# Kernel tuning notes

Measured on AMD Instinct MI355X. Metric: run time of the kernel, lower is better.

Reference implementation:

```python
import jax, jax.numpy as jnp
import numpy as np
from jax import lax

R = 1          # box-filter radius
EPS = 1e-06    # regularizer


def boxfilter(z, r=R):
    """ReplicationPad2d(r) + depthwise (groups=C) mean conv with kernel (2r+1)^2."""
    k = 2 * r + 1
    c = z.shape[1]
    zp = jnp.pad(z, ((0, 0), (0, 0), (r, r), (r, r)), mode='edge')  # replication pad
    w = jnp.full((c, 1, k, k), 1.0 / (k * k), dtype=z.dtype)        # [O, I/g, kh, kw]
    return lax.conv_general_dilated(zp, w, window_strides=(1, 1), padding='VALID',
                                    feature_group_count=c)


def setup_inputs() -> dict:
    key = jax.random.key(0)
    kx, ky = jax.random.split(key)
    shape = (8, 3, 1024, 1024)
    # image-valued inputs in [0, 255), matching the final clamp range
    x = jax.random.uniform(kx, shape, jnp.float32, 0.0, 255.0)
    y = jax.random.uniform(ky, shape, jnp.float32, 0.0, 255.0)
    return {"x": x, "y": y}


def reference(x, y):
    mean_x = boxfilter(x)
    mean_y = boxfilter(y)
    cov_xy = boxfilter(x * y) - mean_x * mean_y
    var_x = boxfilter(x * x) - mean_x * mean_x
    A = cov_xy / (var_x + EPS)
    b = mean_y - A * mean_x
    res = boxfilter(A) * x + boxfilter(b)
    # torch: res.int() truncates toward zero, clamp(0,255), back to float
    return jnp.clip(jnp.trunc(res), 0.0, 255.0)
```

## Files before the change

kernel.cpp:

```cpp
#include <hip/hip_runtime.h>


#define TW 64
#define TH 16

__global__ __launch_bounds__(256) void gf_kernel(
    const float* __restrict__ x, const float* __restrict__ y,
    float* __restrict__ out, int H, int W) {
  const int img = blockIdx.z;
  const size_t base = (size_t)img * H * W;
  const int tx0 = blockIdx.x * TW;
  const int ty0 = blockIdx.y * TH;

  __shared__ float sx[TH + 4][TW + 4];
  __shared__ float sy[TH + 4][TW + 4];
  __shared__ float sA[TH + 2][TW + 2];
  __shared__ float sB[TH + 2][TW + 2];

  const int tid = threadIdx.y * 64 + threadIdx.x;

  for (int i = tid; i < (TH + 4) * (TW + 4); i += 256) {
    int ly = i / (TW + 4);
    int lx = i - ly * (TW + 4);
    int gy = min(max(ty0 + ly - 2, 0), H - 1);
    int gx = min(max(tx0 + lx - 2, 0), W - 1);
    size_t g = base + (size_t)gy * W + gx;
    sx[ly][lx] = x[g];
    sy[ly][lx] = y[g];
  }
  __syncthreads();

  const float inv9 = 1.0f / 9.0f;
  for (int i = tid; i < (TH + 2) * (TW + 2); i += 256) {
    int ly = i / (TW + 2);
    int lx = i - ly * (TW + 2);
    int cy = min(max(ty0 + ly - 1, 0), H - 1);
    int cx = min(max(tx0 + lx - 1, 0), W - 1);
    int sy0 = cy - ty0 + 2;
    int sx0 = cx - tx0 + 2;
    float Sx = 0.f, Sy = 0.f, Sxy = 0.f, Sxx = 0.f;
#pragma unroll
    for (int dy = -1; dy <= 1; ++dy)
#pragma unroll
      for (int dx = -1; dx <= 1; ++dx) {
        float vx = sx[sy0 + dy][sx0 + dx];
        float vy = sy[sy0 + dy][sx0 + dx];
        Sx += vx;
        Sy += vy;
        Sxy += vx * vy;
        Sxx += vx * vx;
      }
    float mx = Sx * inv9, my = Sy * inv9;
    float cov = Sxy * inv9 - mx * my;
    float var = Sxx * inv9 - mx * mx;
    float A = cov / (var + 1e-6f);
    sA[ly][lx] = A;
    sB[ly][lx] = my - A * mx;
  }
  __syncthreads();

  for (int ry = threadIdx.y; ry < TH; ry += 4) {
    int lx = threadIdx.x;
    float SA = 0.f, SB = 0.f;
#pragma unroll
    for (int dy = 0; dy < 3; ++dy)
#pragma unroll
      for (int dx = 0; dx < 3; ++dx) {
        SA += sA[ry + dy][lx + dx];
        SB += sB[ry + dy][lx + dx];
      }
    float xv = sx[ry + 2][lx + 2];
    float res = SA * inv9 * xv + SB * inv9;
    float t = truncf(res);
    t = fminf(fmaxf(t, 0.0f), 255.0f);
    out[base + (size_t)(ty0 + ry) * W + (tx0 + lx)] = t;
  }
}

extern "C" void kernel_launch(void* const* d_in, const int* in_sizes, int n_in,
                              void* d_out, int out_size, void* d_ws, size_t ws_size,
                              hipStream_t stream) {
  const float* x = (const float*)d_in[0];
  const float* y = (const float*)d_in[1];
  float* out = (float*)d_out;
  const int H = 1024, W = 1024;
  const int imgs = in_sizes[0] / (H * W);
  dim3 block(64, 4, 1);
  dim3 grid(W / TW, H / TH, imgs);
  gf_kernel<<<grid, block, 0, stream>>>(x, y, out, H, W);
}
```

Before: 275.0 us.

## Replace shared-memory tiles with per-wave row-streaming and shuffle-based box filters

Drops the LDS tiles and block-wide barriers. Each 64-lane wave now walks down 32 rows of a 60-column strip, doing the horizontal box sums with lane shuffles and keeping a three-row rolling window of A and b in registers. The exact division is replaced by the hardware reciprocal instruction on a rescaled numerator and denominator, and replication-padding edges are handled with a shuffle fix-up. The cost is redundant global loads (each input row is read three times per step, relying on cache) and overlapping halo columns between strips. The approximate reciprocal also risks rounding differences that could change truncated outputs.

```diff
diff --git a/kernel.cpp b/kernel.cpp
--- a/kernel.cpp
+++ b/kernel.cpp
@@ -1,80 +1,95 @@
 #include <hip/hip_runtime.h>
 
 
-#define TW 64
-#define TH 16
+#define TH 32
+#define OW 60
 
 __global__ __launch_bounds__(256) void gf_kernel(
-    const float* __restrict__ x, const float* __restrict__ y,
-    float* __restrict__ out, int H, int W) {
+    const float* __restrict__ xg, const float* __restrict__ yg,
+    float* __restrict__ outg, int H, int W) {
+  const int lane = threadIdx.x;
   const int img = blockIdx.z;
-  const size_t base = (size_t)img * H * W;
-  const int tx0 = blockIdx.x * TW;
-  const int ty0 = blockIdx.y * TH;
+  const size_t ibase = (size_t)img * H * W;
+  const float* __restrict__ xi = xg + ibase;
+  const float* __restrict__ yi = yg + ibase;
+  float* __restrict__ oi = outg + ibase;
 
-  __shared__ float sx[TH + 4][TW + 4];
-  __shared__ float sy[TH + 4][TW + 4];
-  __shared__ float sA[TH + 2][TW + 2];
-  __shared__ float sB[TH + 2][TW + 2];
+  int tx0 = blockIdx.x * OW;
+  if (tx0 > W - OW) tx0 = W - OW;
+  const int ty0 = (blockIdx.y * 4 + threadIdx.y) * TH;
 
-  const int tid = threadIdx.y * 64 + threadIdx.x;
+  const int col = tx0 + lane - 2;
+  const int gxc = min(max(col, 0), W - 1);
+  const bool wok = (lane >= 2) && (lane < 62);
 
-  for (int i = tid; i < (TH + 4) * (TW + 4); i += 256) {
-    int ly = i / (TW + 4);
-    int lx = i - ly * (TW + 4);
-    int gy = min(max(ty0 + ly - 2, 0), H - 1);
-    int gx = min(max(tx0 + lx - 2, 0), W - 1);
-    size_t g = base + (size_t)gy * W + gx;
-    sx[ly][lx] = x[g];
-    sy[ly][lx] = y[g];
-  }
-  __syncthreads();
+  const bool leftE = (tx0 == 0);
+  const bool rightE = (tx0 + OW >= W);
+  const bool needfix = leftE || rightE;
+  int fixsrc = lane;
+  if (leftE && lane == 1) fixsrc = 2;
+  if (rightE && lane == 62) fixsrc = 61;
 
   const float inv9 = 1.0f / 9.0f;
-  for (int i = tid; i < (TH + 2) * (TW + 2); i += 256) {
-    int ly = i / (TW + 2);
-    int lx = i - ly * (TW + 2);
+
+  float hA0 = 0.f, hA1 = 0.f, hA2 = 0.f;
+  float hB0 = 0.f, hB1 = 0.f, hB2 = 0.f;
+
+  auto step = [&](int ly, bool emit) {
     int cy = min(max(ty0 + ly - 1, 0), H - 1);
-    int cx = min(max(tx0 + lx - 1, 0), W - 1);
-    int sy0 = cy - ty0 + 2;
-    int sx0 = cx - tx0 + 2;
-    float Sx = 0.f, Sy = 0.f, Sxy = 0.f, Sxx = 0.f;
-#pragma unroll
-    for (int dy = -1; dy <= 1; ++dy)
-#pragma unroll
-      for (int dx = -1; dx <= 1; ++dx) {
-        float vx = sx[sy0 + dy][sx0 + dx];
-        float vy = sy[sy0 + dy][sx0 + dx];
-        Sx += vx;
-        Sy += vy;
-        Sxy += vx * vy;
-        Sxx += vx * vx;
-      }
-    float mx = Sx * inv9, my = Sy * inv9;
-    float cov = Sxy * inv9 - mx * my;
-    float var = Sxx * inv9 - mx * mx;
-    float A = cov / (var + 1e-6f);
-    sA[ly][lx] = A;
-    sB[ly][lx] = my - A * mx;
-  }
-  __syncthreads();
+    int r0 = max(cy - 1, 0);
+    int r2 = min(cy + 1, H - 1);
+    const float* xr0 = xi + (size_t)r0 * W;
+    const float* xr1 = xi + (size_t)cy * W;
+    const float* xr2 = xi + (size_t)r2 * W;
+    const float* yr0 = yi + (size_t)r0 * W;
+    const float* yr1 = yi + (size_t)cy * W;
+    const float* yr2 = yi + (size_t)r2 * W;
+    float xa = xr0[gxc], xb = xr1[gxc], xc = xr2[gxc];
+    float ya = yr0[gxc], yb = yr1[gxc], yc = yr2[gxc];
 
-  for (int ry = threadIdx.y; ry < TH; ry += 4) {
-    int lx = threadIdx.x;
-    float SA = 0.f, SB = 0.f;
-#pragma unroll
-    for (int dy = 0; dy < 3; ++dy)
-#pragma unroll
-      for (int dx = 0; dx < 3; ++dx) {
-        SA += sA[ry + dy][lx + dx];
-        SB += sB[ry + dy][lx + dx];
-      }
-    float xv = sx[ry + 2][lx + 2];
-    float res = SA * inv9 * xv + SB * inv9;
-    float t = truncf(res);
-    t = fminf(fmaxf(t, 0.0f), 255.0f);
-    out[base + (size_t)(ty0 + ry) * W + (tx0 + lx)] = t;
-  }
+    float vx = xa + xb + xc;
+    float vy = ya + yb + yc;
+    float vxy = xa * ya + xb * yb + xc * yc;
+    float vxx = xa * xa + xb * xb + xc * xc;
+
+    float Sx  = __shfl_up(vx, 1)  + vx  + __shfl_down(vx, 1);
+    float Sy  = __shfl_up(vy, 1)  + vy  + __shfl_down(vy, 1);
+    float Sxy = __shfl_up(vxy, 1) + vxy + __shfl_down(vxy, 1);
+    float Sxx = __shfl_up(vxx, 1) + vxx + __shfl_down(vxx, 1);
+
+    float num = 9.0f * Sxy - Sx * Sy;
+    float den = 9.0f * Sxx - Sx * Sx + 8.1e-05f;
+    float rden;
+    asm("v_rcp_f32 %0, %1" : "=v"(rden) : "v"(den));
+    float A = num * rden;
+    float b = Sy * inv9 - A * (Sx * inv9);
+
+    if (needfix) {
+      A = __shfl(A, fixsrc);
+      b = __shfl(b, fixsrc);
+    }
+
+    float hAn = __shfl_up(A, 1) + A + __shfl_down(A, 1);
+    float hBn = __shfl_up(b, 1) + b + __shfl_down(b, 1);
+    hA0 = hA1; hA1 = hA2; hA2 = hAn;
+    hB0 = hB1; hB1 = hB2; hB2 = hBn;
+
+    if (emit) {
+      int gr = ty0 + ly - 2;
+      float xv = (r0 == gr) ? xa : xb;
+      float SA = hA0 + hA1 + hA2;
+      float SB = hB0 + hB1 + hB2;
+      float res = (SA * xv + SB) * inv9;
+      float t = truncf(res);
+      t = fminf(fmaxf(t, 0.0f), 255.0f);
+      if (wok) oi[(size_t)gr * W + col] = t;
+    }
+  };
+
+  step(0, false);
+  step(1, false);
+#pragma unroll 4
+  for (int ly = 2; ly < TH + 2; ++ly) step(ly, true);
 }
 
 extern "C" void kernel_launch(void* const* d_in, const int* in_sizes, int n_in,
@@ -86,6 +101,6 @@
   const int H = 1024, W = 1024;
   const int imgs = in_sizes[0] / (H * W);
   dim3 block(64, 4, 1);
-  dim3 grid(W / TW, H / TH, imgs);
+  dim3 grid((W + OW - 1) / OW, H / (TH * 4), imgs);
   gf_kernel<<<grid, block, 0, stream>>>(x, y, out, H, W);
 }
```

Result: slower. 297.1 us (+8.0%).
